# Performance work log

Measured on AMD Instinct MI355X. Metric: run time of the kernel, lower is better.

## Reference

```python
import jax, jax.numpy as jnp
import numpy as np

B, H = 8192, 768


def _mk_linear(key, fan_in, fan_out):
    k1, k2 = jax.random.split(key)
    lim = 1.0 / np.sqrt(fan_in)
    W = jax.random.uniform(k1, (fan_out, fan_in), jnp.float32, -lim, lim)
    b = jax.random.uniform(k2, (fan_out,), jnp.float32, -lim, lim)
    return W, b


def setup_inputs() -> dict:
    key = jax.random.key(0)
    ks = jax.random.split(key, 6)
    modal_a = jax.random.normal(ks[0], (B, H), jnp.float32)
    modal_b = jax.random.normal(ks[1], (B, H), jnp.float32)
    W1m, b1m = _mk_linear(ks[2], H, H)
    W2m, b2m = _mk_linear(ks[3], H, H)
    W1v, b1v = _mk_linear(ks[4], H, H)
    W2v, b2v = _mk_linear(ks[5], H, H)
    return {"modal_a": modal_a, "modal_b": modal_b,
            "W1m": W1m, "b1m": b1m, "W2m": W2m, "b2m": b2m,
            "W1v": W1v, "b1v": b1v, "W2v": W2v, "b2v": b2v}


def reference(modal_a, modal_b, W1m, b1m, W2m, b2m, W1v, b1v, W2v, b2v):
    # mlp_mu: Linear -> Tanh -> Linear
    mu = jnp.tanh(modal_a @ W1m.T + b1m) @ W2m.T + b2m              # [B,H]
    # mlp_logvar: Linear -> Tanh -> Linear -> Tanh
    logvar = jnp.tanh(jnp.tanh(modal_a @ W1v.T + b1v) @ W2v.T + b2v)  # [B,H]
    inv_var = jnp.exp(-logvar)

    positive = -(mu - modal_b) ** 2 * 0.5 * inv_var                  # [B,H]

    # mean_j (mu[j] - mu[i])^2 = E[mu^2] - 2*mu[i]*E[mu] + mu[i]^2  (per feature dim)
    # Algebraic reduction of the O(B^2*H) tile in the original code.
    mu_mean = jnp.mean(mu, axis=0)                                   # [H]
    mu_sq_mean = jnp.mean(mu * mu, axis=0)                           # [H]
    pair_sq = mu_sq_mean - 2.0 * mu * mu_mean + mu * mu              # [B,H]
    negative = -pair_sq * 0.5 * inv_var                              # [B,H]

    pos_sum = jnp.sum(positive, axis=-1)                             # [B]
    neg_sum = jnp.sum(negative, axis=-1)                             # [B]
    lld = jnp.mean(pos_sum)
    bound = jnp.mean(pos_sum - neg_sum)
    return (lld, bound)
```

## Files before the change

### kernel.cpp

```cpp
#include <hip/hip_runtime.h>
#include <hip/hip_fp8.h>
#include <math.h>

typedef float v4f __attribute__((ext_vector_type(4)));

#define AS1 __attribute__((address_space(1)))
#define AS3 __attribute__((address_space(3)))

static constexpr int Bn = 8192;
static constexpr int Hn = 768;
static constexpr float invB = 1.0f / 8192.0f;

__device__ __forceinline__ unsigned char cvt_e4m3(float x) {
    __hip_fp8_e4m3 t(x);
    return t.__x;
}

__device__ __forceinline__ float fast_tanh(float x) {
    float xc = fminf(fmaxf(x, -15.0f), 15.0f);
    float e = __expf(2.0f * xc);
    float r = __builtin_amdgcn_rcpf(e + 1.0f);
    return 1.0f - 2.0f * r;
}

__global__ void prep_kernel(const float* __restrict__ A,
                            const float* __restrict__ W1m, const float* __restrict__ W2m,
                            const float* __restrict__ W1v, const float* __restrict__ W2v,
                            unsigned char* __restrict__ A_f8,
                            unsigned char* __restrict__ W1m_f8, unsigned char* __restrict__ W2m_f8,
                            unsigned char* __restrict__ W1v_f8, unsigned char* __restrict__ W2v_f8,
                            float* __restrict__ zbuf, int nzero) {
    const int tid = blockIdx.x * blockDim.x + threadIdx.x;
    if (tid < nzero) zbuf[tid] = 0.0f;
    constexpr int A4 = Bn * Hn / 4;
    constexpr int W4 = Hn * Hn / 4;
    const int total = A4 + 4 * W4;
    const int stride = gridDim.x * blockDim.x;
    for (int i = tid; i < total; i += stride) {
        const float* s; unsigned char* d; int j;
        if (i < A4) { s = A; d = A_f8; j = i; }
        else {
            int k = i - A4; int w = k / W4; j = k - w * W4;
            s = (w == 0) ? W1m : (w == 1) ? W2m : (w == 2) ? W1v : W2v;
            d = (w == 0) ? W1m_f8 : (w == 1) ? W2m_f8 : (w == 2) ? W1v_f8 : W2v_f8;
        }
        float4 v = ((const float4*)s)[j];
        unsigned p = (unsigned)cvt_e4m3(v.x)
                   | ((unsigned)cvt_e4m3(v.y) << 8)
                   | ((unsigned)cvt_e4m3(v.z) << 16)
                   | ((unsigned)cvt_e4m3(v.w) << 24);
        ((unsigned*)d)[j] = p;
    }
}

__launch_bounds__(256, 2)
__global__ void gemm_l1(const unsigned char* __restrict__ A_g,
                        const unsigned char* __restrict__ Wm_g, const unsigned char* __restrict__ Wv_g,
                        const float* __restrict__ bm, const float* __restrict__ bv,
                        unsigned char* __restrict__ outm, unsigned char* __restrict__ outv) {
    __shared__ __align__(16) unsigned char smem[49152];
    unsigned char* As  = smem;
    unsigned char* Wms = smem + 16384;
    unsigned char* Wvs = smem + 32768;

    const int t = threadIdx.x;
    const int row0 = blockIdx.x * 128;
    const int col0 = blockIdx.y * 128;
    const int w = t >> 6, lane = t & 63;
    const int wm = w >> 1, wn = w & 1;
    const int lr = lane & 15, quad = lane >> 4;
    const int q2 = quad >> 1, q1 = quad & 1;

    const int rst = t >> 3, cst = t & 7;
    const int csrc = cst ^ (rst & 7);

    const unsigned char* pA[4]; const unsigned char* pWm[4]; const unsigned char* pWv[4];
#pragma unroll
    for (int i = 0; i < 4; ++i) {
        pA[i]  = A_g  + (size_t)(row0 + i * 32 + rst) * Hn + csrc * 16;
        pWm[i] = Wm_g + (size_t)(col0 + i * 32 + rst) * Hn + csrc * 16;
        pWv[i] = Wv_g + (size_t)(col0 + i * 32 + rst) * Hn + csrc * 16;
    }

    v4f accm[4][4] = {}, accv[4][4] = {};

    for (int k0 = 0; k0 < Hn; k0 += 128) {
#pragma unroll
        for (int i = 0; i < 4; ++i) {
            __builtin_amdgcn_global_load_lds((AS1 void*)pA[i],  (AS3 void*)&As[i * 4096 + t * 16], 16, 0, 0);
            __builtin_amdgcn_global_load_lds((AS1 void*)pWm[i], (AS3 void*)&Wms[i * 4096 + t * 16], 16, 0, 0);
            __builtin_amdgcn_global_load_lds((AS1 void*)pWv[i], (AS3 void*)&Wvs[i * 4096 + t * 16], 16, 0, 0);
            pA[i] += 128; pWm[i] += 128; pWv[i] += 128;
        }
        __syncthreads();
#pragma unroll
        for (int ks = 0; ks < 4; ++ks) {
            const int cg = ks * 2 + q2;
            long fb[4], fam[4], fav[4];
#pragma unroll
            for (int mt = 0; mt < 4; ++mt) {
                int m = wm * 64 + mt * 16 + lr;
                fb[mt] = *(const long*)&As[m * 128 + ((cg ^ (m & 7)) << 4) + (q1 << 3)];
            }
#pragma unroll
            for (int nt = 0; nt < 4; ++nt) {
                int n = wn * 64 + nt * 16 + lr;
                int off = n * 128 + ((cg ^ (n & 7)) << 4) + (q1 << 3);
                fam[nt] = *(const long*)&Wms[off];
                fav[nt] = *(const long*)&Wvs[off];
            }
#pragma unroll
            for (int nt = 0; nt < 4; ++nt)
#pragma unroll
                for (int mt = 0; mt < 4; ++mt) {
                    accm[nt][mt] = __builtin_amdgcn_mfma_f32_16x16x32_fp8_fp8(fam[nt], fb[mt], accm[nt][mt], 0, 0, 0);
                    accv[nt][mt] = __builtin_amdgcn_mfma_f32_16x16x32_fp8_fp8(fav[nt], fb[mt], accv[nt][mt], 0, 0, 0);
                }
        }
        __syncthreads();
    }

    unsigned* sm32 = (unsigned*)smem;
#pragma unroll
    for (int br = 0; br < 2; ++br) {
        const float* bias = br ? bv : bm;
        unsigned char* out = br ? outv : outm;
#pragma unroll
        for (int nt = 0; nt < 4; ++nt) {
            float4 bb = *(const float4*)&bias[col0 + wn * 64 + nt * 16 + quad * 4];
#pragma unroll
            for (int mt = 0; mt < 4; ++mt) {
                const int row_l = wm * 64 + mt * 16 + lr;
                v4f a = br ? accv[nt][mt] : accm[nt][mt];
                unsigned p = (unsigned)cvt_e4m3(fast_tanh(a[0] + bb.x))
                           | ((unsigned)cvt_e4m3(fast_tanh(a[1] + bb.y)) << 8)
                           | ((unsigned)cvt_e4m3(fast_tanh(a[2] + bb.z)) << 16)
                           | ((unsigned)cvt_e4m3(fast_tanh(a[3] + bb.w)) << 24);
                sm32[row_l * 36 + wn * 16 + nt * 4 + quad] = p;
            }
        }
        __syncthreads();
#pragma unroll
        for (int i = 0; i < 4; ++i) {
            const int idx = i * 256 + t;
            const int row = idx >> 3, seg = idx & 7;
            uint4 d = *(const uint4*)&sm32[row * 36 + seg * 4];
            *(uint4*)&out[(size_t)(row0 + row) * Hn + col0 + seg * 16] = d;
        }
        __syncthreads();
    }
}

__launch_bounds__(256, 2)
__global__ void gemm_l2(const unsigned char* __restrict__ Am_g, const unsigned char* __restrict__ Av_g,
                        const unsigned char* __restrict__ Wm_g, const unsigned char* __restrict__ Wv_g,
                        const float* __restrict__ bm, const float* __restrict__ bv,
                        const float* __restrict__ mb,
                        float* __restrict__ cs, float* __restrict__ cs2,
                        float* __restrict__ siv, float* __restrict__ sivmu,
                        float* __restrict__ accum, float* __restrict__ outp) {
    __shared__ __align__(16) unsigned char smem[65536];
    unsigned char* Ams = smem;
    unsigned char* Avs = smem + 16384;
    unsigned char* Wms = smem + 32768;
    unsigned char* Wvs = smem + 49152;

    const int t = threadIdx.x;
    const int row0 = blockIdx.x * 128;
    const int col0 = blockIdx.y * 128;
    const int w = t >> 6, lane = t & 63;
    const int wm = w >> 1, wn = w & 1;
    const int lr = lane & 15, quad = lane >> 4;
    const int q2 = quad >> 1, q1 = quad & 1;

    const int rst = t >> 3, cst = t & 7;
    const int csrc = cst ^ (rst & 7);

    const unsigned char* pAm[4]; const unsigned char* pAv[4];
    const unsigned char* pWm[4]; const unsigned char* pWv[4];
#pragma unroll
    for (int i = 0; i < 4; ++i) {
        pAm[i] = Am_g + (size_t)(row0 + i * 32 + rst) * Hn + csrc * 16;
        pAv[i] = Av_g + (size_t)(row0 + i * 32 + rst) * Hn + csrc * 16;
        pWm[i] = Wm_g + (size_t)(col0 + i * 32 + rst) * Hn + csrc * 16;
        pWv[i] = Wv_g + (size_t)(col0 + i * 32 + rst) * Hn + csrc * 16;
    }

    v4f accm[4][4] = {}, accv[4][4] = {};

    for (int k0 = 0; k0 < Hn; k0 += 128) {
#pragma unroll
        for (int i = 0; i < 4; ++i) {
            __builtin_amdgcn_global_load_lds((AS1 void*)pAm[i], (AS3 void*)&Ams[i * 4096 + t * 16], 16, 0, 0);
            __builtin_amdgcn_global_load_lds((AS1 void*)pAv[i], (AS3 void*)&Avs[i * 4096 + t * 16], 16, 0, 0);
            __builtin_amdgcn_global_load_lds((AS1 void*)pWm[i], (AS3 void*)&Wms[i * 4096 + t * 16], 16, 0, 0);
            __builtin_amdgcn_global_load_lds((AS1 void*)pWv[i], (AS3 void*)&Wvs[i * 4096 + t * 16], 16, 0, 0);
            pAm[i] += 128; pAv[i] += 128; pWm[i] += 128; pWv[i] += 128;
        }
        __syncthreads();
#pragma unroll
        for (int ks = 0; ks < 4; ++ks) {
            const int cg = ks * 2 + q2;
            long fam[4], fav[4], fwm[4], fwv[4];
#pragma unroll
            for (int mt = 0; mt < 4; ++mt) {
                int m = wm * 64 + mt * 16 + lr;
                int off = m * 128 + ((cg ^ (m & 7)) << 4) + (q1 << 3);
                fam[mt] = *(const long*)&Ams[off];
                fav[mt] = *(const long*)&Avs[off];
            }
#pragma unroll
            for (int nt = 0; nt < 4; ++nt) {
                int n = wn * 64 + nt * 16 + lr;
                int off = n * 128 + ((cg ^ (n & 7)) << 4) + (q1 << 3);
                fwm[nt] = *(const long*)&Wms[off];
                fwv[nt] = *(const long*)&Wvs[off];
            }
#pragma unroll
            for (int mt = 0; mt < 4; ++mt)
#pragma unroll
                for (int nt = 0; nt < 4; ++nt) {
                    accm[mt][nt] = __builtin_amdgcn_mfma_f32_16x16x32_fp8_fp8(fam[mt], fwm[nt], accm[mt][nt], 0, 0, 0);
                    accv[mt][nt] = __builtin_amdgcn_mfma_f32_16x16x32_fp8_fp8(fav[mt], fwv[nt], accv[mt][nt], 0, 0, 0);
                }
        }
        __syncthreads();
    }

    float pos = 0.f, q = 0.f;
#pragma unroll
    for (int nt = 0; nt < 4; ++nt) {
        const int col = col0 + wn * 64 + nt * 16 + lr;
        const float bmc = bm[col], bvc = bv[col];
        float c1 = 0.f, c2 = 0.f, c3 = 0.f, c4 = 0.f;
#pragma unroll
        for (int mt = 0; mt < 4; ++mt) {
#pragma unroll
            for (int r = 0; r < 4; ++r) {
                const int row = row0 + wm * 64 + mt * 16 + quad * 4 + r;
                float mu = accm[mt][nt][r] + bmc;
                float tv = fast_tanh(accv[mt][nt][r] + bvc);
                float iv = __expf(-tv);
                float mbv = mb[(size_t)row * Hn + col];
                float d = mu - mbv;
                pos += iv * d * d;
                q   += iv * mu * mu;
                c1 += mu; c2 += mu * mu; c3 += iv; c4 += iv * mu;
            }
        }
        c1 += __shfl_xor(c1, 16); c1 += __shfl_xor(c1, 32);
        c2 += __shfl_xor(c2, 16); c2 += __shfl_xor(c2, 32);
        c3 += __shfl_xor(c3, 16); c3 += __shfl_xor(c3, 32);
        c4 += __shfl_xor(c4, 16); c4 += __shfl_xor(c4, 32);
        if (quad == 0) {
            atomicAdd(&cs[col], c1);
            atomicAdd(&cs2[col], c2);
            atomicAdd(&siv[col], c3);
            atomicAdd(&sivmu[col], c4);
        }
    }
    for (int off = 32; off > 0; off >>= 1) {
        pos += __shfl_down(pos, off);
        q   += __shfl_down(q, off);
    }
    __shared__ float redP[4], redQ[4];
    if (lane == 0) { redP[w] = pos; redQ[w] = q; }
    __syncthreads();
    __shared__ int is_last;
    if (t == 0) {
        atomicAdd(&accum[0], redP[0] + redP[1] + redP[2] + redP[3]);
        atomicAdd(&accum[1], redQ[0] + redQ[1] + redQ[2] + redQ[3]);
        __threadfence();
        unsigned old = atomicAdd((unsigned int*)&accum[3], 1u);
        is_last = (old == gridDim.x * gridDim.y - 1) ? 1 : 0;
    }
    __syncthreads();
    if (is_last) {
        float term = 0.f;
        for (int h = t; h < Hn; h += 256) {
            float v1 = atomicAdd(&cs[h], 0.0f);
            float v2 = atomicAdd(&cs2[h], 0.0f);
            float v3 = atomicAdd(&siv[h], 0.0f);
            float v4 = atomicAdd(&sivmu[h], 0.0f);
            term += v3 * v2 - 2.0f * v4 * v1;
        }
        for (int off = 32; off > 0; off >>= 1) term += __shfl_down(term, off);
        __shared__ float redT[4];
        if (lane == 0) redT[w] = term;
        __syncthreads();
        if (t == 0) {
            float T = redT[0] + redT[1] + redT[2] + redT[3];
            float P = atomicAdd(&accum[0], 0.0f);
            float Q = atomicAdd(&accum[1], 0.0f);
            float pos_sum = -0.5f * P;
            float neg_sum = -0.5f * (T * invB + Q);
            outp[0] = pos_sum * invB;
            outp[1] = (pos_sum - neg_sum) * invB;
        }
    }
}

extern "C" void kernel_launch(void* const* d_in, const int* in_sizes, int n_in,
                              void* d_out, int out_size, void* d_ws, size_t ws_size,
                              hipStream_t stream) {
    const float* modal_a = (const float*)d_in[0];
    const float* modal_b = (const float*)d_in[1];
    const float* W1m = (const float*)d_in[2];
    const float* b1m = (const float*)d_in[3];
    const float* W2m = (const float*)d_in[4];
    const float* b2m = (const float*)d_in[5];
    const float* W1v = (const float*)d_in[6];
    const float* b1v = (const float*)d_in[7];
    const float* W2v = (const float*)d_in[8];
    const float* b2v = (const float*)d_in[9];
    float* out = (float*)d_out;

    char* ws = (char*)d_ws;
    constexpr size_t szA8 = (size_t)Bn * Hn;
    constexpr size_t szW8 = (size_t)Hn * Hn;
    unsigned char* A_f8   = (unsigned char*)(ws);
    unsigned char* h1m_f8 = (unsigned char*)(ws + szA8);
    unsigned char* h1v_f8 = (unsigned char*)(ws + 2 * szA8);
    unsigned char* W1m_f8 = (unsigned char*)(ws + 3 * szA8);
    unsigned char* W2m_f8 = (unsigned char*)(ws + 3 * szA8 + szW8);
    unsigned char* W1v_f8 = (unsigned char*)(ws + 3 * szA8 + 2 * szW8);
    unsigned char* W2v_f8 = (unsigned char*)(ws + 3 * szA8 + 3 * szW8);
    float* cs     = (float*)(ws + 3 * szA8 + 4 * szW8);
    float* cs2    = cs + Hn;
    float* siv    = cs + 2 * Hn;
    float* sivmu  = cs + 3 * Hn;
    float* accum  = cs + 4 * Hn;

    prep_kernel<<<1280, 256, 0, stream>>>(modal_a, W1m, W2m, W1v, W2v,
                                          A_f8, W1m_f8, W2m_f8, W1v_f8, W2v_f8,
                                          cs, 4 * Hn + 8);

    gemm_l1<<<dim3(Bn / 128, Hn / 128), 256, 0, stream>>>(
        A_f8, W1m_f8, W1v_f8, b1m, b1v, h1m_f8, h1v_f8);

    gemm_l2<<<dim3(Bn / 128, Hn / 128), 256, 0, stream>>>(
        h1m_f8, h1v_f8, W2m_f8, W2v_f8, b2m, b2v, modal_b,
        cs, cs2, siv, sivmu, accum, out);
}
```

Measured before the change: 176.3 us.

## Double-buffer K=64 stages in both GEMMs and split L1 branches across grid z

Both fp8 GEMM kernels now stream K in 64-wide stages into two LDS buffers, issuing the next stage's global-to-LDS loads before computing the current one and gating on vmcnt, instead of loading a full 128-K tile and synchronising each iteration. gemm_l1 computes only one branch (mu or logvar) per block via blockIdx.z, doubling the grid and halving accumulators and LDS. gemm_l2 uses 64-row tiles so it launches twice as many blocks. Smaller footprints let launch bounds ask for 3 blocks per CU. The cost is that gemm_l1 now loads each A tile twice, and there are more barriers per K.

```diff
diff --git a/kernel.cpp b/kernel.cpp
--- a/kernel.cpp
+++ b/kernel.cpp
@@ -53,105 +53,143 @@
     }
 }
 
-__launch_bounds__(256, 2)
+__device__ __forceinline__ int swz4(int r) { return (r ^ (r >> 2)) & 3; }
+
+__device__ __forceinline__ void l1_compute(const unsigned char* bb_,
+                                           int wm, int wn, int lr, int q1, int q2,
+                                           v4f acc[4][4]) {
+#pragma unroll
+    for (int ks = 0; ks < 2; ++ks) {
+        const int cg = ks * 2 + q2;
+        long fb[4], fa[4];
+#pragma unroll
+        for (int mt = 0; mt < 4; ++mt) {
+            int m = wm * 64 + mt * 16 + lr;
+            fb[mt] = *(const long*)&bb_[m * 64 + ((cg ^ swz4(m)) << 4) + (q1 << 3)];
+        }
+#pragma unroll
+        for (int nt = 0; nt < 4; ++nt) {
+            int n = wn * 64 + nt * 16 + lr;
+            fa[nt] = *(const long*)&bb_[8192 + n * 64 + ((cg ^ swz4(n)) << 4) + (q1 << 3)];
+        }
+#pragma unroll
+        for (int nt = 0; nt < 4; ++nt)
+#pragma unroll
+            for (int mt = 0; mt < 4; ++mt)
+                acc[nt][mt] = __builtin_amdgcn_mfma_f32_16x16x32_fp8_fp8(fa[nt], fb[mt], acc[nt][mt], 0, 0, 0);
+    }
+}
+
+__launch_bounds__(256, 3)
 __global__ void gemm_l1(const unsigned char* __restrict__ A_g,
                         const unsigned char* __restrict__ Wm_g, const unsigned char* __restrict__ Wv_g,
                         const float* __restrict__ bm, const float* __restrict__ bv,
                         unsigned char* __restrict__ outm, unsigned char* __restrict__ outv) {
-    __shared__ __align__(16) unsigned char smem[49152];
-    unsigned char* As  = smem;
-    unsigned char* Wms = smem + 16384;
-    unsigned char* Wvs = smem + 32768;
-
+    __shared__ __align__(16) unsigned char smem[32768];
     const int t = threadIdx.x;
     const int row0 = blockIdx.x * 128;
     const int col0 = blockIdx.y * 128;
+    const int br = blockIdx.z;
+    const unsigned char* Wg = br ? Wv_g : Wm_g;
+    const float* bias = br ? bv : bm;
+    unsigned char* out = br ? outv : outm;
+
     const int w = t >> 6, lane = t & 63;
     const int wm = w >> 1, wn = w & 1;
     const int lr = lane & 15, quad = lane >> 4;
     const int q2 = quad >> 1, q1 = quad & 1;
 
-    const int rst = t >> 3, cst = t & 7;
-    const int csrc = cst ^ (rst & 7);
-
-    const unsigned char* pA[4]; const unsigned char* pWm[4]; const unsigned char* pWv[4];
+    const int rst = t >> 2, cst = t & 3;
+    const int csrc = cst ^ swz4(rst);
+
+    const unsigned char* sA = A_g + (size_t)(row0 + rst) * Hn + csrc * 16;
+    const unsigned char* sW = Wg  + (size_t)(col0 + rst) * Hn + csrc * 16;
+
+    v4f acc[4][4] = {};
+
+#define L1_STAGE(h_, nb_) do {                                                                                   \
+    const int kb_ = (h_) * 64;                                                                                   \
+    unsigned char* db_ = smem + (nb_) * 16384;                                                                   \
+    __builtin_amdgcn_global_load_lds((const AS1 void*)(sA + kb_),           (AS3 void*)(db_ + t * 16), 16, 0, 0);          \
+    __builtin_amdgcn_global_load_lds((const AS1 void*)(sA + 64 * Hn + kb_), (AS3 void*)(db_ + 4096 + t * 16), 16, 0, 0);   \
+    __builtin_amdgcn_global_load_lds((const AS1 void*)(sW + kb_),           (AS3 void*)(db_ + 8192 + t * 16), 16, 0, 0);   \
+    __builtin_amdgcn_global_load_lds((const AS1 void*)(sW + 64 * Hn + kb_), (AS3 void*)(db_ + 12288 + t * 16), 16, 0, 0);  \
+  } while (0)
+
+    L1_STAGE(0, 0);
+    for (int h = 0; h < 11; ++h) {
+        L1_STAGE(h + 1, (h + 1) & 1);
+        asm volatile("s_waitcnt vmcnt(4)" ::: "memory");
+        __builtin_amdgcn_s_barrier();
+        __builtin_amdgcn_sched_barrier(0);
+        l1_compute(smem + (h & 1) * 16384, wm, wn, lr, q1, q2, acc);
+        __builtin_amdgcn_sched_barrier(0);
+        __builtin_amdgcn_s_barrier();
+    }
+    asm volatile("s_waitcnt vmcnt(0)" ::: "memory");
+    __builtin_amdgcn_s_barrier();
+    __builtin_amdgcn_sched_barrier(0);
+    l1_compute(smem + 16384, wm, wn, lr, q1, q2, acc);
+    __syncthreads();
+#undef L1_STAGE
+
+    unsigned* sm32 = (unsigned*)smem;
+#pragma unroll
+    for (int nt = 0; nt < 4; ++nt) {
+        float4 bb = *(const float4*)&bias[col0 + wn * 64 + nt * 16 + quad * 4];
+#pragma unroll
+        for (int mt = 0; mt < 4; ++mt) {
+            const int row_l = wm * 64 + mt * 16 + lr;
+            v4f a = acc[nt][mt];
+            unsigned p = (unsigned)cvt_e4m3(fast_tanh(a[0] + bb.x))
+                       | ((unsigned)cvt_e4m3(fast_tanh(a[1] + bb.y)) << 8)
+                       | ((unsigned)cvt_e4m3(fast_tanh(a[2] + bb.z)) << 16)
+                       | ((unsigned)cvt_e4m3(fast_tanh(a[3] + bb.w)) << 24);
+            sm32[row_l * 36 + wn * 16 + nt * 4 + quad] = p;
+        }
+    }
+    __syncthreads();
 #pragma unroll
     for (int i = 0; i < 4; ++i) {
-        pA[i]  = A_g  + (size_t)(row0 + i * 32 + rst) * Hn + csrc * 16;
-        pWm[i] = Wm_g + (size_t)(col0 + i * 32 + rst) * Hn + csrc * 16;
-        pWv[i] = Wv_g + (size_t)(col0 + i * 32 + rst) * Hn + csrc * 16;
-    }
-
-    v4f accm[4][4] = {}, accv[4][4] = {};
-
-    for (int k0 = 0; k0 < Hn; k0 += 128) {
-#pragma unroll
-        for (int i = 0; i < 4; ++i) {
-            __builtin_amdgcn_global_load_lds((AS1 void*)pA[i],  (AS3 void*)&As[i * 4096 + t * 16], 16, 0, 0);
-            __builtin_amdgcn_global_load_lds((AS1 void*)pWm[i], (AS3 void*)&Wms[i * 4096 + t * 16], 16, 0, 0);
-            __builtin_amdgcn_global_load_lds((AS1 void*)pWv[i], (AS3 void*)&Wvs[i * 4096 + t * 16], 16, 0, 0);
-            pA[i] += 128; pWm[i] += 128; pWv[i] += 128;
-        }
-        __syncthreads();
-#pragma unroll
-        for (int ks = 0; ks < 4; ++ks) {
-            const int cg = ks * 2 + q2;
-            long fb[4], fam[4], fav[4];
-#pragma unroll
-            for (int mt = 0; mt < 4; ++mt) {
-                int m = wm * 64 + mt * 16 + lr;
-                fb[mt] = *(const long*)&As[m * 128 + ((cg ^ (m & 7)) << 4) + (q1 << 3)];
+        const int idx = i * 256 + t;
+        const int row = idx >> 3, seg = idx & 7;
+        uint4 d = *(const uint4*)&sm32[row * 36 + seg * 4];
+        *(uint4*)&out[(size_t)(row0 + row) * Hn + col0 + seg * 16] = d;
+    }
+}
+
+__device__ __forceinline__ void l2_compute(const unsigned char* bb_,
+                                           int wm, int wn, int lr, int q1, int q2,
+                                           v4f accm[2][4], v4f accv[2][4]) {
+#pragma unroll
+    for (int ks = 0; ks < 2; ++ks) {
+        const int cg = ks * 2 + q2;
+        long fam[2], fav[2], fwm[4], fwv[4];
+#pragma unroll
+        for (int mt = 0; mt < 2; ++mt) {
+            int m = wm * 32 + mt * 16 + lr;
+            int off = m * 64 + ((cg ^ swz4(m)) << 4) + (q1 << 3);
+            fam[mt] = *(const long*)&bb_[off];
+            fav[mt] = *(const long*)&bb_[4096 + off];
+        }
+#pragma unroll
+        for (int nt = 0; nt < 4; ++nt) {
+            int n = wn * 64 + nt * 16 + lr;
+            int off = n * 64 + ((cg ^ swz4(n)) << 4) + (q1 << 3);
+            fwm[nt] = *(const long*)&bb_[8192 + off];
+            fwv[nt] = *(const long*)&bb_[16384 + off];
+        }
+#pragma unroll
+        for (int mt = 0; mt < 2; ++mt)
+#pragma unroll
+            for (int nt = 0; nt < 4; ++nt) {
+                accm[mt][nt] = __builtin_amdgcn_mfma_f32_16x16x32_fp8_fp8(fam[mt], fwm[nt], accm[mt][nt], 0, 0, 0);
+                accv[mt][nt] = __builtin_amdgcn_mfma_f32_16x16x32_fp8_fp8(fav[mt], fwv[nt], accv[mt][nt], 0, 0, 0);
             }
-#pragma unroll
-            for (int nt = 0; nt < 4; ++nt) {
-                int n = wn * 64 + nt * 16 + lr;
-                int off = n * 128 + ((cg ^ (n & 7)) << 4) + (q1 << 3);
-                fam[nt] = *(const long*)&Wms[off];
-                fav[nt] = *(const long*)&Wvs[off];
-            }
-#pragma unroll
-            for (int nt = 0; nt < 4; ++nt)
-#pragma unroll
-                for (int mt = 0; mt < 4; ++mt) {
-                    accm[nt][mt] = __builtin_amdgcn_mfma_f32_16x16x32_fp8_fp8(fam[nt], fb[mt], accm[nt][mt], 0, 0, 0);
-                    accv[nt][mt] = __builtin_amdgcn_mfma_f32_16x16x32_fp8_fp8(fav[nt], fb[mt], accv[nt][mt], 0, 0, 0);
-                }
-        }
-        __syncthreads();
-    }
-
-    unsigned* sm32 = (unsigned*)smem;
-#pragma unroll
-    for (int br = 0; br < 2; ++br) {
-        const float* bias = br ? bv : bm;
-        unsigned char* out = br ? outv : outm;
-#pragma unroll
-        for (int nt = 0; nt < 4; ++nt) {
-            float4 bb = *(const float4*)&bias[col0 + wn * 64 + nt * 16 + quad * 4];
-#pragma unroll
-            for (int mt = 0; mt < 4; ++mt) {
-                const int row_l = wm * 64 + mt * 16 + lr;
-                v4f a = br ? accv[nt][mt] : accm[nt][mt];
-                unsigned p = (unsigned)cvt_e4m3(fast_tanh(a[0] + bb.x))
-                           | ((unsigned)cvt_e4m3(fast_tanh(a[1] + bb.y)) << 8)
-                           | ((unsigned)cvt_e4m3(fast_tanh(a[2] + bb.z)) << 16)
-                           | ((unsigned)cvt_e4m3(fast_tanh(a[3] + bb.w)) << 24);
-                sm32[row_l * 36 + wn * 16 + nt * 4 + quad] = p;
-            }
-        }
-        __syncthreads();
-#pragma unroll
-        for (int i = 0; i < 4; ++i) {
-            const int idx = i * 256 + t;
-            const int row = idx >> 3, seg = idx & 7;
-            uint4 d = *(const uint4*)&sm32[row * 36 + seg * 4];
-            *(uint4*)&out[(size_t)(row0 + row) * Hn + col0 + seg * 16] = d;
-        }
-        __syncthreads();
-    }
-}
-
-__launch_bounds__(256, 2)
+    }
+}
+
+__launch_bounds__(256, 3)
 __global__ void gemm_l2(const unsigned char* __restrict__ Am_g, const unsigned char* __restrict__ Av_g,
                         const unsigned char* __restrict__ Wm_g, const unsigned char* __restrict__ Wv_g,
                         const float* __restrict__ bm, const float* __restrict__ bv,
@@ -159,73 +197,51 @@
                         float* __restrict__ cs, float* __restrict__ cs2,
                         float* __restrict__ siv, float* __restrict__ sivmu,
                         float* __restrict__ accum, float* __restrict__ outp) {
-    __shared__ __align__(16) unsigned char smem[65536];
-    unsigned char* Ams = smem;
-    unsigned char* Avs = smem + 16384;
-    unsigned char* Wms = smem + 32768;
-    unsigned char* Wvs = smem + 49152;
-
+    __shared__ __align__(16) unsigned char smem[49152];
     const int t = threadIdx.x;
-    const int row0 = blockIdx.x * 128;
+    const int row0 = blockIdx.x * 64;
     const int col0 = blockIdx.y * 128;
     const int w = t >> 6, lane = t & 63;
     const int wm = w >> 1, wn = w & 1;
     const int lr = lane & 15, quad = lane >> 4;
     const int q2 = quad >> 1, q1 = quad & 1;
 
-    const int rst = t >> 3, cst = t & 7;
-    const int csrc = cst ^ (rst & 7);
-
-    const unsigned char* pAm[4]; const unsigned char* pAv[4];
-    const unsigned char* pWm[4]; const unsigned char* pWv[4];
-#pragma unroll
-    for (int i = 0; i < 4; ++i) {
-        pAm[i] = Am_g + (size_t)(row0 + i * 32 + rst) * Hn + csrc * 16;
-        pAv[i] = Av_g + (size_t)(row0 + i * 32 + rst) * Hn + csrc * 16;
-        pWm[i] = Wm_g + (size_t)(col0 + i * 32 + rst) * Hn + csrc * 16;
-        pWv[i] = Wv_g + (size_t)(col0 + i * 32 + rst) * Hn + csrc * 16;
-    }
-
-    v4f accm[4][4] = {}, accv[4][4] = {};
-
-    for (int k0 = 0; k0 < Hn; k0 += 128) {
-#pragma unroll
-        for (int i = 0; i < 4; ++i) {
-            __builtin_amdgcn_global_load_lds((AS1 void*)pAm[i], (AS3 void*)&Ams[i * 4096 + t * 16], 16, 0, 0);
-            __builtin_amdgcn_global_load_lds((AS1 void*)pAv[i], (AS3 void*)&Avs[i * 4096 + t * 16], 16, 0, 0);
-            __builtin_amdgcn_global_load_lds((AS1 void*)pWm[i], (AS3 void*)&Wms[i * 4096 + t * 16], 16, 0, 0);
-            __builtin_amdgcn_global_load_lds((AS1 void*)pWv[i], (AS3 void*)&Wvs[i * 4096 + t * 16], 16, 0, 0);
-            pAm[i] += 128; pAv[i] += 128; pWm[i] += 128; pWv[i] += 128;
-        }
-        __syncthreads();
-#pragma unroll
-        for (int ks = 0; ks < 4; ++ks) {
-            const int cg = ks * 2 + q2;
-            long fam[4], fav[4], fwm[4], fwv[4];
-#pragma unroll
-            for (int mt = 0; mt < 4; ++mt) {
-                int m = wm * 64 + mt * 16 + lr;
-                int off = m * 128 + ((cg ^ (m & 7)) << 4) + (q1 << 3);
-                fam[mt] = *(const long*)&Ams[off];
-                fav[mt] = *(const long*)&Avs[off];
-            }
-#pragma unroll
-            for (int nt = 0; nt < 4; ++nt) {
-                int n = wn * 64 + nt * 16 + lr;
-                int off = n * 128 + ((cg ^ (n & 7)) << 4) + (q1 << 3);
-                fwm[nt] = *(const long*)&Wms[off];
-                fwv[nt] = *(const long*)&Wvs[off];
-            }
-#pragma unroll
-            for (int mt = 0; mt < 4; ++mt)
-#pragma unroll
-                for (int nt = 0; nt < 4; ++nt) {
-                    accm[mt][nt] = __builtin_amdgcn_mfma_f32_16x16x32_fp8_fp8(fam[mt], fwm[nt], accm[mt][nt], 0, 0, 0);
-                    accv[mt][nt] = __builtin_amdgcn_mfma_f32_16x16x32_fp8_fp8(fav[mt], fwv[nt], accv[mt][nt], 0, 0, 0);
-                }
-        }
-        __syncthreads();
-    }
+    const int rst = t >> 2, cst = t & 3;
+    const int csrc = cst ^ swz4(rst);
+
+    const unsigned char* sAm = Am_g + (size_t)(row0 + rst) * Hn + csrc * 16;
+    const unsigned char* sAv = Av_g + (size_t)(row0 + rst) * Hn + csrc * 16;
+    const unsigned char* sWm = Wm_g + (size_t)(col0 + rst) * Hn + csrc * 16;
+    const unsigned char* sWv = Wv_g + (size_t)(col0 + rst) * Hn + csrc * 16;
+
+    v4f accm[2][4] = {}, accv[2][4] = {};
+
+#define L2_STAGE(h_, nb_) do {                                                                                    \
+    const int kb_ = (h_) * 64;                                                                                    \
+    unsigned char* db_ = smem + (nb_) * 24576;                                                                    \
+    __builtin_amdgcn_global_load_lds((const AS1 void*)(sAm + kb_),           (AS3 void*)(db_ + t * 16), 16, 0, 0);          \
+    __builtin_amdgcn_global_load_lds((const AS1 void*)(sAv + kb_),           (AS3 void*)(db_ + 4096 + t * 16), 16, 0, 0);   \
+    __builtin_amdgcn_global_load_lds((const AS1 void*)(sWm + kb_),           (AS3 void*)(db_ + 8192 + t * 16), 16, 0, 0);   \
+    __builtin_amdgcn_global_load_lds((const AS1 void*)(sWm + 64 * Hn + kb_), (AS3 void*)(db_ + 12288 + t * 16), 16, 0, 0);  \
+    __builtin_amdgcn_global_load_lds((const AS1 void*)(sWv + kb_),           (AS3 void*)(db_ + 16384 + t * 16), 16, 0, 0);  \
+    __builtin_amdgcn_global_load_lds((const AS1 void*)(sWv + 64 * Hn + kb_), (AS3 void*)(db_ + 20480 + t * 16), 16, 0, 0);  \
+  } while (0)
+
+    L2_STAGE(0, 0);
+    for (int h = 0; h < 11; ++h) {
+        L2_STAGE(h + 1, (h + 1) & 1);
+        asm volatile("s_waitcnt vmcnt(6)" ::: "memory");
+        __builtin_amdgcn_s_barrier();
+        __builtin_amdgcn_sched_barrier(0);
+        l2_compute(smem + (h & 1) * 24576, wm, wn, lr, q1, q2, accm, accv);
+        __builtin_amdgcn_sched_barrier(0);
+        __builtin_amdgcn_s_barrier();
+    }
+    asm volatile("s_waitcnt vmcnt(0)" ::: "memory");
+    __builtin_amdgcn_s_barrier();
+    __builtin_amdgcn_sched_barrier(0);
+    l2_compute(smem + 24576, wm, wn, lr, q1, q2, accm, accv);
+#undef L2_STAGE
 
     float pos = 0.f, q = 0.f;
 #pragma unroll
@@ -234,10 +250,10 @@
         const float bmc = bm[col], bvc = bv[col];
         float c1 = 0.f, c2 = 0.f, c3 = 0.f, c4 = 0.f;
 #pragma unroll
-        for (int mt = 0; mt < 4; ++mt) {
+        for (int mt = 0; mt < 2; ++mt) {
 #pragma unroll
             for (int r = 0; r < 4; ++r) {
-                const int row = row0 + wm * 64 + mt * 16 + quad * 4 + r;
+                const int row = row0 + wm * 32 + mt * 16 + quad * 4 + r;
                 float mu = accm[mt][nt][r] + bmc;
                 float tv = fast_tanh(accv[mt][nt][r] + bvc);
                 float iv = __expf(-tv);
@@ -335,10 +351,10 @@
                                           A_f8, W1m_f8, W2m_f8, W1v_f8, W2v_f8,
                                           cs, 4 * Hn + 8);
 
-    gemm_l1<<<dim3(Bn / 128, Hn / 128), 256, 0, stream>>>(
+    gemm_l1<<<dim3(Bn / 128, Hn / 128, 2), 256, 0, stream>>>(
         A_f8, W1m_f8, W1v_f8, b1m, b1v, h1m_f8, h1v_f8);
 
-    gemm_l2<<<dim3(Bn / 128, Hn / 128), 256, 0, stream>>>(
+    gemm_l2<<<dim3(Bn / 64, Hn / 128), 256, 0, stream>>>(
         h1m_f8, h1v_f8, W2m_f8, W2v_f8, b2m, b2v, modal_b,
         cs, cs2, siv, sivmu, accum, out);
 }
```

New measurement: 178.2 us. About the same (+1.1%).

## Restructure FP8 GEMMs into full-row strips with weights streamed from global

Applied to the files above, without the earlier changes.

Both GEMM kernels now stage a full-width activation strip (64 or 32 rows by 768) in shared memory once. Each of 8 waves streams its own 96 weight columns straight from global/L2 into registers, double-buffered across K steps, instead of tiling 128x128 with per-K shared-memory staging and barriers. This removes the per-K-step syncthreads and the shared-memory staging of weights, and lets layer 1 write its whole output row tile contiguously. The trade-off is that weights are re-read from L2 by every block, and register pressure is higher with 512-thread blocks.

```diff
diff --git a/kernel.cpp b/kernel.cpp
--- a/kernel.cpp
+++ b/kernel.cpp
@@ -3,9 +3,6 @@
 #include <math.h>
 
 typedef float v4f __attribute__((ext_vector_type(4)));
-
-#define AS1 __attribute__((address_space(1)))
-#define AS3 __attribute__((address_space(3)))
 
 static constexpr int Bn = 8192;
 static constexpr int Hn = 768;
@@ -53,193 +50,185 @@
     }
 }
 
-__launch_bounds__(256, 2)
+
+__launch_bounds__(512, 2)
 __global__ void gemm_l1(const unsigned char* __restrict__ A_g,
                         const unsigned char* __restrict__ Wm_g, const unsigned char* __restrict__ Wv_g,
                         const float* __restrict__ bm, const float* __restrict__ bv,
                         unsigned char* __restrict__ outm, unsigned char* __restrict__ outv) {
-    __shared__ __align__(16) unsigned char smem[49152];
-    unsigned char* As  = smem;
-    unsigned char* Wms = smem + 16384;
-    unsigned char* Wvs = smem + 32768;
-
+    __shared__ __align__(16) unsigned char As[64 * 768];
     const int t = threadIdx.x;
-    const int row0 = blockIdx.x * 128;
-    const int col0 = blockIdx.y * 128;
+    const int strip0 = blockIdx.x * 64;
+    const int br = blockIdx.y;
+    const unsigned char* __restrict__ Wg = br ? Wv_g : Wm_g;
+    const float* __restrict__ bias = br ? bv : bm;
+    unsigned char* __restrict__ out = br ? outv : outm;
+
+    {
+        const int row = t >> 3, c8 = t & 7;
+        const unsigned char* src = A_g + (size_t)(strip0 + row) * Hn + c8 * 16;
+        unsigned char* dst = As + row * 768;
+#pragma unroll
+        for (int j = 0; j < 6; ++j) {
+            const int c = c8 + 8 * j;
+            uint4 v = *(const uint4*)(src + j * 128);
+            *(uint4*)(dst + ((c ^ (row & 7)) << 4)) = v;
+        }
+    }
+    __syncthreads();
+
     const int w = t >> 6, lane = t & 63;
-    const int wm = w >> 1, wn = w & 1;
     const int lr = lane & 15, quad = lane >> 4;
-    const int q2 = quad >> 1, q1 = quad & 1;
-
-    const int rst = t >> 3, cst = t & 7;
-    const int csrc = cst ^ (rst & 7);
-
-    const unsigned char* pA[4]; const unsigned char* pWm[4]; const unsigned char* pWv[4];
-#pragma unroll
-    for (int i = 0; i < 4; ++i) {
-        pA[i]  = A_g  + (size_t)(row0 + i * 32 + rst) * Hn + csrc * 16;
-        pWm[i] = Wm_g + (size_t)(col0 + i * 32 + rst) * Hn + csrc * 16;
-        pWv[i] = Wv_g + (size_t)(col0 + i * 32 + rst) * Hn + csrc * 16;
-    }
-
-    v4f accm[4][4] = {}, accv[4][4] = {};
-
-    for (int k0 = 0; k0 < Hn; k0 += 128) {
-#pragma unroll
-        for (int i = 0; i < 4; ++i) {
-            __builtin_amdgcn_global_load_lds((AS1 void*)pA[i],  (AS3 void*)&As[i * 4096 + t * 16], 16, 0, 0);
-            __builtin_amdgcn_global_load_lds((AS1 void*)pWm[i], (AS3 void*)&Wms[i * 4096 + t * 16], 16, 0, 0);
-            __builtin_amdgcn_global_load_lds((AS1 void*)pWv[i], (AS3 void*)&Wvs[i * 4096 + t * 16], 16, 0, 0);
-            pA[i] += 128; pWm[i] += 128; pWv[i] += 128;
-        }
-        __syncthreads();
-#pragma unroll
-        for (int ks = 0; ks < 4; ++ks) {
-            const int cg = ks * 2 + q2;
-            long fb[4], fam[4], fav[4];
-#pragma unroll
-            for (int mt = 0; mt < 4; ++mt) {
-                int m = wm * 64 + mt * 16 + lr;
-                fb[mt] = *(const long*)&As[m * 128 + ((cg ^ (m & 7)) << 4) + (q1 << 3)];
-            }
-#pragma unroll
-            for (int nt = 0; nt < 4; ++nt) {
-                int n = wn * 64 + nt * 16 + lr;
-                int off = n * 128 + ((cg ^ (n & 7)) << 4) + (q1 << 3);
-                fam[nt] = *(const long*)&Wms[off];
-                fav[nt] = *(const long*)&Wvs[off];
-            }
-#pragma unroll
-            for (int nt = 0; nt < 4; ++nt)
-#pragma unroll
-                for (int mt = 0; mt < 4; ++mt) {
-                    accm[nt][mt] = __builtin_amdgcn_mfma_f32_16x16x32_fp8_fp8(fam[nt], fb[mt], accm[nt][mt], 0, 0, 0);
-                    accv[nt][mt] = __builtin_amdgcn_mfma_f32_16x16x32_fp8_fp8(fav[nt], fb[mt], accv[nt][mt], 0, 0, 0);
-                }
-        }
-        __syncthreads();
-    }
-
-    unsigned* sm32 = (unsigned*)smem;
-#pragma unroll
-    for (int br = 0; br < 2; ++br) {
-        const float* bias = br ? bv : bm;
-        unsigned char* out = br ? outv : outm;
-#pragma unroll
-        for (int nt = 0; nt < 4; ++nt) {
-            float4 bb = *(const float4*)&bias[col0 + wn * 64 + nt * 16 + quad * 4];
-#pragma unroll
-            for (int mt = 0; mt < 4; ++mt) {
-                const int row_l = wm * 64 + mt * 16 + lr;
-                v4f a = br ? accv[nt][mt] : accm[nt][mt];
-                unsigned p = (unsigned)cvt_e4m3(fast_tanh(a[0] + bb.x))
-                           | ((unsigned)cvt_e4m3(fast_tanh(a[1] + bb.y)) << 8)
-                           | ((unsigned)cvt_e4m3(fast_tanh(a[2] + bb.z)) << 16)
-                           | ((unsigned)cvt_e4m3(fast_tanh(a[3] + bb.w)) << 24);
-                sm32[row_l * 36 + wn * 16 + nt * 4 + quad] = p;
-            }
-        }
-        __syncthreads();
-#pragma unroll
-        for (int i = 0; i < 4; ++i) {
-            const int idx = i * 256 + t;
-            const int row = idx >> 3, seg = idx & 7;
-            uint4 d = *(const uint4*)&sm32[row * 36 + seg * 4];
-            *(uint4*)&out[(size_t)(row0 + row) * Hn + col0 + seg * 16] = d;
-        }
-        __syncthreads();
-    }
-}
-
-__launch_bounds__(256, 2)
-__global__ void gemm_l2(const unsigned char* __restrict__ Am_g, const unsigned char* __restrict__ Av_g,
+    const int wc0 = w * 96;
+
+    const unsigned char* __restrict__ pW = Wg + (size_t)(wc0 + lr) * Hn + quad * 16;
+
+    v4f acc[6][4] = {};
+    ulonglong2 Wf[2][6], Af[2][4];
+
+#define L1_LOADS(s_, ms_) do {                                                              \
+    _Pragma("unroll")                                                                       \
+    for (int ct = 0; ct < 6; ++ct)                                                          \
+        Wf[s_][ct] = *(const ulonglong2*)(pW + ct * (16 * Hn) + (ms_) * 64);                \
+    _Pragma("unroll")                                                                       \
+    for (int rt = 0; rt < 4; ++rt) {                                                        \
+        const int row_ = rt * 16 + lr;                                                      \
+        const int slot_ = ((ms_) * 4 + quad) ^ (row_ & 7);                                  \
+        Af[s_][rt] = *(const ulonglong2*)&As[row_ * 768 + slot_ * 16];                      \
+    } } while (0)
+
+#define L1_MFMA(s_) do {                                                                    \
+    _Pragma("unroll")                                                                       \
+    for (int ct = 0; ct < 6; ++ct)                                                          \
+    _Pragma("unroll")                                                                       \
+    for (int rt = 0; rt < 4; ++rt) {                                                        \
+        acc[ct][rt] = __builtin_amdgcn_mfma_f32_16x16x32_fp8_fp8((long)Wf[s_][ct].x, (long)Af[s_][rt].x, acc[ct][rt], 0, 0, 0); \
+        acc[ct][rt] = __builtin_amdgcn_mfma_f32_16x16x32_fp8_fp8((long)Wf[s_][ct].y, (long)Af[s_][rt].y, acc[ct][rt], 0, 0, 0); \
+    } } while (0)
+
+    L1_LOADS(0, 0);
+#pragma unroll
+    for (int ms = 0; ms < 12; ++ms) {
+        if (ms < 11) {
+            if ((ms & 1) == 0) L1_LOADS(1, ms + 1); else L1_LOADS(0, ms + 1);
+        }
+        if ((ms & 1) == 0) L1_MFMA(0); else L1_MFMA(1);
+    }
+#undef L1_LOADS
+#undef L1_MFMA
+
+    __syncthreads();
+#pragma unroll
+    for (int ct = 0; ct < 6; ++ct) {
+        const float4 bb = *(const float4*)&bias[wc0 + ct * 16 + quad * 4];
+        const int c = w * 6 + ct;
+#pragma unroll
+        for (int rt = 0; rt < 4; ++rt) {
+            const int row = rt * 16 + lr;
+            v4f a = acc[ct][rt];
+            unsigned p = (unsigned)cvt_e4m3(fast_tanh(a[0] + bb.x))
+                       | ((unsigned)cvt_e4m3(fast_tanh(a[1] + bb.y)) << 8)
+                       | ((unsigned)cvt_e4m3(fast_tanh(a[2] + bb.z)) << 16)
+                       | ((unsigned)cvt_e4m3(fast_tanh(a[3] + bb.w)) << 24);
+            *(unsigned*)&As[row * 768 + ((c ^ (row & 7)) << 4) + quad * 4] = p;
+        }
+    }
+    __syncthreads();
+#pragma unroll
+    for (int i = 0; i < 6; ++i) {
+        const int u = i * 512 + t;
+        const int row = u / 48, c = u - row * 48;
+        uint4 v = *(const uint4*)&As[row * 768 + ((c ^ (row & 7)) << 4)];
+        *(uint4*)&out[(size_t)(strip0 + row) * Hn + c * 16] = v;
+    }
+}
+
+__device__ __forceinline__ void l2_gemm(const unsigned char* Hsrc, const unsigned char* pW,
+                                        int lr, int quad, v4f acc[2][6]) {
+    ulonglong2 Wf[2][6], Af[2][2];
+#define L2_LOADS(s_, ms_) do {                                                              \
+    _Pragma("unroll")                                                                       \
+    for (int ct = 0; ct < 6; ++ct)                                                          \
+        Wf[s_][ct] = *(const ulonglong2*)(pW + ct * (16 * Hn) + (ms_) * 64);                \
+    _Pragma("unroll")                                                                       \
+    for (int rt = 0; rt < 2; ++rt) {                                                        \
+        const int row_ = rt * 16 + lr;                                                      \
+        const int slot_ = ((ms_) * 4 + quad) ^ (row_ & 7);                                  \
+        Af[s_][rt] = *(const ulonglong2*)&Hsrc[row_ * 768 + slot_ * 16];                    \
+    } } while (0)
+
+#define L2_MFMA(s_) do {                                                                    \
+    _Pragma("unroll")                                                                       \
+    for (int rt = 0; rt < 2; ++rt)                                                          \
+    _Pragma("unroll")                                                                       \
+    for (int ct = 0; ct < 6; ++ct) {                                                        \
+        acc[rt][ct] = __builtin_amdgcn_mfma_f32_16x16x32_fp8_fp8((long)Af[s_][rt].x, (long)Wf[s_][ct].x, acc[rt][ct], 0, 0, 0); \
+        acc[rt][ct] = __builtin_amdgcn_mfma_f32_16x16x32_fp8_fp8((long)Af[s_][rt].y, (long)Wf[s_][ct].y, acc[rt][ct], 0, 0, 0); \
+    } } while (0)
+
+    L2_LOADS(0, 0);
+#pragma unroll
+    for (int ms = 0; ms < 12; ++ms) {
+        if (ms < 11) {
+            if ((ms & 1) == 0) L2_LOADS(1, ms + 1); else L2_LOADS(0, ms + 1);
+        }
+        if ((ms & 1) == 0) L2_MFMA(0); else L2_MFMA(1);
+    }
+#undef L2_LOADS
+#undef L2_MFMA
+}
+
+__launch_bounds__(512, 2)
+__global__ void gemm_l2(const unsigned char* __restrict__ h1m_g, const unsigned char* __restrict__ h1v_g,
                         const unsigned char* __restrict__ Wm_g, const unsigned char* __restrict__ Wv_g,
                         const float* __restrict__ bm, const float* __restrict__ bv,
                         const float* __restrict__ mb,
                         float* __restrict__ cs, float* __restrict__ cs2,
                         float* __restrict__ siv, float* __restrict__ sivmu,
                         float* __restrict__ accum, float* __restrict__ outp) {
-    __shared__ __align__(16) unsigned char smem[65536];
-    unsigned char* Ams = smem;
-    unsigned char* Avs = smem + 16384;
-    unsigned char* Wms = smem + 32768;
-    unsigned char* Wvs = smem + 49152;
-
+    __shared__ __align__(16) unsigned char Hs[2][32 * 768];
     const int t = threadIdx.x;
-    const int row0 = blockIdx.x * 128;
-    const int col0 = blockIdx.y * 128;
+    const int strip0 = blockIdx.x * 32;
+
+    {
+        const int row = t >> 4, c16 = t & 15;
+        const size_t goff = (size_t)(strip0 + row) * Hn + c16 * 16;
+#pragma unroll
+        for (int b = 0; b < 2; ++b) {
+            const unsigned char* src = (b ? h1v_g : h1m_g) + goff;
+            unsigned char* dst = Hs[b] + row * 768;
+#pragma unroll
+            for (int j = 0; j < 3; ++j) {
+                const int c = c16 + 16 * j;
+                uint4 v = *(const uint4*)(src + j * 256);
+                *(uint4*)(dst + ((c ^ (row & 7)) << 4)) = v;
+            }
+        }
+    }
+    __syncthreads();
+
     const int w = t >> 6, lane = t & 63;
-    const int wm = w >> 1, wn = w & 1;
     const int lr = lane & 15, quad = lane >> 4;
-    const int q2 = quad >> 1, q1 = quad & 1;
-
-    const int rst = t >> 3, cst = t & 7;
-    const int csrc = cst ^ (rst & 7);
-
-    const unsigned char* pAm[4]; const unsigned char* pAv[4];
-    const unsigned char* pWm[4]; const unsigned char* pWv[4];
-#pragma unroll
-    for (int i = 0; i < 4; ++i) {
-        pAm[i] = Am_g + (size_t)(row0 + i * 32 + rst) * Hn + csrc * 16;
-        pAv[i] = Av_g + (size_t)(row0 + i * 32 + rst) * Hn + csrc * 16;
-        pWm[i] = Wm_g + (size_t)(col0 + i * 32 + rst) * Hn + csrc * 16;
-        pWv[i] = Wv_g + (size_t)(col0 + i * 32 + rst) * Hn + csrc * 16;
-    }
-
-    v4f accm[4][4] = {}, accv[4][4] = {};
-
-    for (int k0 = 0; k0 < Hn; k0 += 128) {
-#pragma unroll
-        for (int i = 0; i < 4; ++i) {
-            __builtin_amdgcn_global_load_lds((AS1 void*)pAm[i], (AS3 void*)&Ams[i * 4096 + t * 16], 16, 0, 0);
-            __builtin_amdgcn_global_load_lds((AS1 void*)pAv[i], (AS3 void*)&Avs[i * 4096 + t * 16], 16, 0, 0);
-            __builtin_amdgcn_global_load_lds((AS1 void*)pWm[i], (AS3 void*)&Wms[i * 4096 + t * 16], 16, 0, 0);
-            __builtin_amdgcn_global_load_lds((AS1 void*)pWv[i], (AS3 void*)&Wvs[i * 4096 + t * 16], 16, 0, 0);
-            pAm[i] += 128; pAv[i] += 128; pWm[i] += 128; pWv[i] += 128;
-        }
-        __syncthreads();
-#pragma unroll
-        for (int ks = 0; ks < 4; ++ks) {
-            const int cg = ks * 2 + q2;
-            long fam[4], fav[4], fwm[4], fwv[4];
-#pragma unroll
-            for (int mt = 0; mt < 4; ++mt) {
-                int m = wm * 64 + mt * 16 + lr;
-                int off = m * 128 + ((cg ^ (m & 7)) << 4) + (q1 << 3);
-                fam[mt] = *(const long*)&Ams[off];
-                fav[mt] = *(const long*)&Avs[off];
-            }
-#pragma unroll
-            for (int nt = 0; nt < 4; ++nt) {
-                int n = wn * 64 + nt * 16 + lr;
-                int off = n * 128 + ((cg ^ (n & 7)) << 4) + (q1 << 3);
-                fwm[nt] = *(const long*)&Wms[off];
-                fwv[nt] = *(const long*)&Wvs[off];
-            }
-#pragma unroll
-            for (int mt = 0; mt < 4; ++mt)
-#pragma unroll
-                for (int nt = 0; nt < 4; ++nt) {
-                    accm[mt][nt] = __builtin_amdgcn_mfma_f32_16x16x32_fp8_fp8(fam[mt], fwm[nt], accm[mt][nt], 0, 0, 0);
-                    accv[mt][nt] = __builtin_amdgcn_mfma_f32_16x16x32_fp8_fp8(fav[mt], fwv[nt], accv[mt][nt], 0, 0, 0);
-                }
-        }
-        __syncthreads();
-    }
+    const int wc0 = w * 96;
+
+    v4f am[2][6] = {}, av[2][6] = {};
+
+    l2_gemm(&Hs[0][0], Wm_g + (size_t)(wc0 + lr) * Hn + quad * 16, lr, quad, am);
+    l2_gemm(&Hs[1][0], Wv_g + (size_t)(wc0 + lr) * Hn + quad * 16, lr, quad, av);
 
     float pos = 0.f, q = 0.f;
 #pragma unroll
-    for (int nt = 0; nt < 4; ++nt) {
-        const int col = col0 + wn * 64 + nt * 16 + lr;
+    for (int ct = 0; ct < 6; ++ct) {
+        const int col = wc0 + ct * 16 + lr;
         const float bmc = bm[col], bvc = bv[col];
         float c1 = 0.f, c2 = 0.f, c3 = 0.f, c4 = 0.f;
 #pragma unroll
-        for (int mt = 0; mt < 4; ++mt) {
+        for (int rt = 0; rt < 2; ++rt) {
 #pragma unroll
             for (int r = 0; r < 4; ++r) {
-                const int row = row0 + wm * 64 + mt * 16 + quad * 4 + r;
-                float mu = accm[mt][nt][r] + bmc;
-                float tv = fast_tanh(accv[mt][nt][r] + bvc);
+                const int row = strip0 + rt * 16 + quad * 4 + r;
+                float mu = am[rt][ct][r] + bmc;
+                float tv = fast_tanh(av[rt][ct][r] + bvc);
                 float iv = __expf(-tv);
                 float mbv = mb[(size_t)row * Hn + col];
                 float d = mu - mbv;
@@ -263,13 +252,16 @@
         pos += __shfl_down(pos, off);
         q   += __shfl_down(q, off);
     }
-    __shared__ float redP[4], redQ[4];
+    __shared__ float redP[8], redQ[8];
     if (lane == 0) { redP[w] = pos; redQ[w] = q; }
     __syncthreads();
     __shared__ int is_last;
     if (t == 0) {
-        atomicAdd(&accum[0], redP[0] + redP[1] + redP[2] + redP[3]);
-        atomicAdd(&accum[1], redQ[0] + redQ[1] + redQ[2] + redQ[3]);
+        float sp = 0.f, sq = 0.f;
+#pragma unroll
+        for (int i = 0; i < 8; ++i) { sp += redP[i]; sq += redQ[i]; }
+        atomicAdd(&accum[0], sp);
+        atomicAdd(&accum[1], sq);
         __threadfence();
         unsigned old = atomicAdd((unsigned int*)&accum[3], 1u);
         is_last = (old == gridDim.x * gridDim.y - 1) ? 1 : 0;
@@ -277,7 +269,7 @@
     __syncthreads();
     if (is_last) {
         float term = 0.f;
-        for (int h = t; h < Hn; h += 256) {
+        for (int h = t; h < Hn; h += 512) {
             float v1 = atomicAdd(&cs[h], 0.0f);
             float v2 = atomicAdd(&cs2[h], 0.0f);
             float v3 = atomicAdd(&siv[h], 0.0f);
@@ -285,11 +277,13 @@
             term += v3 * v2 - 2.0f * v4 * v1;
         }
         for (int off = 32; off > 0; off >>= 1) term += __shfl_down(term, off);
-        __shared__ float redT[4];
+        __shared__ float redT[8];
         if (lane == 0) redT[w] = term;
         __syncthreads();
         if (t == 0) {
-            float T = redT[0] + redT[1] + redT[2] + redT[3];
+            float T = 0.f;
+#pragma unroll
+            for (int i = 0; i < 8; ++i) T += redT[i];
             float P = atomicAdd(&accum[0], 0.0f);
             float Q = atomicAdd(&accum[1], 0.0f);
             float pos_sum = -0.5f * P;
@@ -335,10 +329,10 @@
                                           A_f8, W1m_f8, W2m_f8, W1v_f8, W2v_f8,
                                           cs, 4 * Hn + 8);
 
-    gemm_l1<<<dim3(Bn / 128, Hn / 128), 256, 0, stream>>>(
+    gemm_l1<<<dim3(Bn / 64, 2), 512, 0, stream>>>(
         A_f8, W1m_f8, W1v_f8, b1m, b1v, h1m_f8, h1v_f8);
 
-    gemm_l2<<<dim3(Bn / 128, Hn / 128), 256, 0, stream>>>(
+    gemm_l2<<<dim3(Bn / 32), 512, 0, stream>>>(
         h1m_f8, h1v_f8, W2m_f8, W2v_f8, b2m, b2v, modal_b,
         cs, cs2, siv, sivmu, accum, out);
 }
```

Result: slower. 190.2 us (+7.9%).
